# Kernel optimization log

Measured on AMD Instinct MI355X. Metric: run time of the kernel, lower is better.

The kernel has to match this reference:

```python
import jax, jax.numpy as jnp
import numpy as np

B, S, H, D = 8, 1024, 1024, 64

def setup_inputs() -> dict:
    key = jax.random.key(0)
    ks = jax.random.split(key, 8)
    return {
        "query": jax.random.normal(ks[0], (B, S, H), jnp.float32),
        "key": jax.random.normal(ks[1], (B, S, H), jnp.float32),
        "value": jax.random.normal(ks[2], (B, S, H), jnp.float32),
        "Wq": jax.random.normal(ks[3], (H, D), jnp.float32) * 0.02,
        "bq": jnp.zeros((D,), jnp.float32),
        "Wk": jax.random.normal(ks[4], (H, D), jnp.float32) * 0.02,
        "bk": jnp.zeros((D,), jnp.float32),
        "Wv": jax.random.normal(ks[5], (H, D), jnp.float32) * 0.02,
        "bv": jnp.zeros((D,), jnp.float32),
        "k_bias_matrix": jax.random.normal(ks[6], (S, S, D), jnp.float32) * 0.02,
        "v_bias_matrix": jax.random.normal(ks[7], (S, S, D), jnp.float32) * 0.02,
        "mask": jnp.ones((B, S), jnp.int32),
    }

def reference(query, key, value, Wq, bq, Wk, bk, Wv, bv, k_bias_matrix, v_bias_matrix, mask):
    # Linear projections: [B,S,H] -> [B,S,D]
    q = query @ Wq + bq
    k = key @ Wk + bk
    v = value @ Wv + bv
    # Standard content score + Shaw relative-position key bias score
    attn_1 = jnp.einsum('bqd,bkd->bqk', q, k)
    attn_2 = jnp.einsum('bqd,qkd->bqk', q, k_bias_matrix)
    scores = (attn_1 + attn_2) / jnp.sqrt(jnp.float32(D))
    scores = jnp.where(mask[:, None, :] == 0, jnp.float32(-1e9), scores)
    w = jax.nn.softmax(scores, axis=-1)  # [B,S,S]
    values_1 = jnp.einsum('bqk,bkd->bqd', w, v)
    values_2 = jnp.einsum('bqk,qkd->bqd', w, v_bias_matrix)
    return values_1 + values_2
```

## Files before the change

### kernel.cpp

```cpp
#include <hip/hip_runtime.h>
#include <hip/hip_bf16.h>
#include <cstdint>
#include <cstddef>

#define NB 8
#define NS 1024
#define NH 1024
#define ND 64

typedef __attribute__((ext_vector_type(8))) short bf8_t;
typedef __attribute__((ext_vector_type(4))) float f32x4;
typedef __attribute__((ext_vector_type(4))) short short4v;

__device__ __forceinline__ short f2bfs(float x) {
    union { __hip_bfloat16 h; short s; } u;
    u.h = __float2bfloat16(x);
    return u.s;
}
__device__ __forceinline__ float bf2f(unsigned short h) {
    return __uint_as_float(((unsigned int)h) << 16);
}
__device__ __forceinline__ bf8_t pack_bf8(float4 a, float4 b) {
    bf8_t r;
    r[0] = f2bfs(a.x); r[1] = f2bfs(a.y); r[2] = f2bfs(a.z); r[3] = f2bfs(a.w);
    r[4] = f2bfs(b.x); r[5] = f2bfs(b.y); r[6] = f2bfs(b.z); r[7] = f2bfs(b.w);
    return r;
}

#define QP_OFF  0
#define KP_OFF  524288
#define VPT_OFF 1048576
#define S1_OFF  1572864
#define WT_OFF  9961472

__global__ __launch_bounds__(256, 8) void wcvt_kernel(
    const float* __restrict__ Wq, const float* __restrict__ Wk,
    const float* __restrict__ Wv, short* __restrict__ wt)
{
    const int p = blockIdx.y;
    const int n = blockIdx.x;
    const float* W = (p == 0) ? Wq : (p == 1) ? Wk : Wv;
    const int k0 = threadIdx.x * 4;
    short4v pk;
    #pragma unroll
    for (int i = 0; i < 4; ++i) pk[i] = f2bfs(W[(size_t)(k0 + i) * ND + n]);
    *(short4v*)&wt[((size_t)p * 64 + n) * 1024 + k0] = pk;
}

__global__ __launch_bounds__(256, 3) void proj_kernel(
    const float* __restrict__ qin, const float* __restrict__ kin, const float* __restrict__ vin,
    const short* __restrict__ wt,
    const float* __restrict__ bq, const float* __restrict__ bk, const float* __restrict__ bv,
    short* __restrict__ ws_s)
{
    __shared__ float red[2][16][68];

    const int p = blockIdx.y;
    const float* A    = (p == 0) ? qin : (p == 1) ? kin : vin;
    const float* bias = (p == 0) ? bq  : (p == 1) ? bk  : bv;

    const int t = threadIdx.x;
    const int wv = t >> 6, l = t & 63, lr = l & 15, lg = l >> 4;
    const int rt = wv >> 1, kh = wv & 1;
    const int rw = blockIdx.x * 32 + rt * 16;

    const short* wtp = wt + ((size_t)p * 64) * 1024 + kh * 512;
    const float* ab  = A + (size_t)(rw + lr) * NH + kh * 512;

    f32x4 acc[4];
    #pragma unroll
    for (int n = 0; n < 4; ++n) acc[n] = (f32x4){0.f, 0.f, 0.f, 0.f};

    #pragma unroll 2
    for (int ch = 0; ch < 4; ++ch) {
        #pragma unroll
        for (int s = 0; s < 4; ++s) {
            const int off = ch * 128 + s * 32 + lg * 8;
            bf8_t af = pack_bf8(*(const float4*)&ab[off], *(const float4*)&ab[off + 4]);
            #pragma unroll
            for (int n = 0; n < 4; ++n) {
                bf8_t bf = *(const bf8_t*)&wtp[(size_t)(n * 16 + lr) * 1024 + off];
                acc[n] = __builtin_amdgcn_mfma_f32_16x16x32_bf16(af, bf, acc[n], 0, 0, 0);
            }
        }
    }

    if (kh) {
        #pragma unroll
        for (int n = 0; n < 4; ++n)
            #pragma unroll
            for (int r = 0; r < 4; ++r)
                red[rt][lg * 4 + r][n * 16 + lr] = acc[n][r];
    }
    __syncthreads();
    if (!kh) {
        if (p < 2) {
            short* dst = ws_s + ((p == 0) ? QP_OFF : KP_OFF);
            const float sc = (p == 0) ? 0.125f : 1.0f;
            #pragma unroll
            for (int n = 0; n < 4; ++n) {
                const float bs = bias[n * 16 + lr];
                #pragma unroll
                for (int r = 0; r < 4; ++r) {
                    float v = acc[n][r] + red[rt][lg * 4 + r][n * 16 + lr] + bs;
                    dst[(size_t)(rw + lg * 4 + r) * ND + n * 16 + lr] = f2bfs(v * sc);
                }
            }
        } else {
            short* vpT = ws_s + VPT_OFF;
            const int b = rw >> 10;
            const int sbase = (rw & 1023) + lg * 4;
            #pragma unroll
            for (int n = 0; n < 4; ++n) {
                const float bs = bias[n * 16 + lr];
                short4v pk;
                #pragma unroll
                for (int r = 0; r < 4; ++r)
                    pk[r] = f2bfs(acc[n][r] + red[rt][lg * 4 + r][n * 16 + lr] + bs);
                *(short4v*)&vpT[((size_t)b * 64 + n * 16 + lr) * NS + sbase] = pk;
            }
        }
    }
}

__global__ __launch_bounds__(256, 4) void scores_c_kernel(
    const short* __restrict__ ws_s, short* __restrict__ s1)
{
    const short* qp = ws_s + QP_OFF;
    const short* kp = ws_s + KP_OFF;
    const int t = threadIdx.x;
    const int wv = t >> 6, l = t & 63, lr = l & 15, lg = l >> 4;
    const int q0 = blockIdx.y * 16;
    const int k0 = blockIdx.x * 64 + wv * 16;

    #pragma unroll
    for (int b = 0; b < 8; ++b) {
        const short* ap = &qp[((size_t)b * NS + q0 + lr) * ND + lg * 8];
        const short* bp = &kp[((size_t)b * NS + k0 + lr) * ND + lg * 8];
        bf8_t a0 = *(const bf8_t*)ap;
        bf8_t a1 = *(const bf8_t*)(ap + 32);
        bf8_t b0 = *(const bf8_t*)bp;
        bf8_t b1 = *(const bf8_t*)(bp + 32);
        f32x4 acc = {0.f, 0.f, 0.f, 0.f};
        acc = __builtin_amdgcn_mfma_f32_16x16x32_bf16(a0, b0, acc, 0, 0, 0);
        acc = __builtin_amdgcn_mfma_f32_16x16x32_bf16(a1, b1, acc, 0, 0, 0);
        #pragma unroll
        for (int r = 0; r < 4; ++r)
            s1[((size_t)b * NS + q0 + lg * 4 + r) * NS + k0 + lr] = f2bfs(acc[r]);
    }
}

__global__ __launch_bounds__(256, 4) void mega_kernel(
    const short* __restrict__ ws_s,
    short* __restrict__ s1,
    const float* __restrict__ kbias,
    const float* __restrict__ vbias,
    const int* __restrict__ mask,
    float* __restrict__ out)
{
    __shared__ __align__(16) short Sb[8][1032];
    __shared__ __align__(16) short WtT[8 * 16 * 64];

    const short* qp = ws_s + QP_OFF;
    const int q = blockIdx.x, t = threadIdx.x;
    const int wv = t >> 6, l = t & 63, lr = l & 15, lg = l >> 4;

    {
        const bf8_t aq0 = *(const bf8_t*)&qp[((size_t)(lr & 7) * NS + q) * ND + lg * 8];
        const bf8_t aq1 = *(const bf8_t*)&qp[((size_t)(lr & 7) * NS + q) * ND + 32 + lg * 8];
        const float* kbq = kbias + (size_t)q * NS * ND;

        #pragma unroll 4
        for (int it = 0; it < 16; ++it) {
            const int k0 = wv * 256 + it * 16;
            const float* kb = &kbq[(size_t)(k0 + lr) * ND + lg * 8];
            bf8_t b0 = pack_bf8(*(const float4*)kb, *(const float4*)(kb + 4));
            bf8_t b1 = pack_bf8(*(const float4*)(kb + 32), *(const float4*)(kb + 36));
            f32x4 acc = {0.f, 0.f, 0.f, 0.f};
            acc = __builtin_amdgcn_mfma_f32_16x16x32_bf16(aq0, b0, acc, 0, 0, 0);
            acc = __builtin_amdgcn_mfma_f32_16x16x32_bf16(aq1, b1, acc, 0, 0, 0);
            if (lg < 2) {
                #pragma unroll
                for (int r = 0; r < 4; ++r)
                    Sb[lg * 4 + r][k0 + lr] = f2bfs(acc[r]);
            }
        }
    }
    __syncthreads();

    {
        const int b = t >> 5, idx = t & 31;
        const int kk = idx * 32;
        short* r1 = s1 + ((size_t)b * NS + q) * NS + kk;
        const int* mb = mask + b * NS + kk;
        const float LOG2E = 1.4426950408889634f;

        float x[32];
        float m = -3.0e38f;
        #pragma unroll
        for (int c = 0; c < 4; ++c) {
            uint4 a4 = *(const uint4*)&r1[8 * c];
            uint4 b4 = *(const uint4*)&Sb[b][kk + 8 * c];
            int4 m0 = *(const int4*)&mb[8 * c];
            int4 m1 = *(const int4*)&mb[8 * c + 4];
            const unsigned short* ap = (const unsigned short*)&a4;
            const unsigned short* bp = (const unsigned short*)&b4;
            const int* mp = (const int*)&m0;
            const int* mq = (const int*)&m1;
            #pragma unroll
            for (int j = 0; j < 8; ++j) {
                float v = bf2f(ap[j]) + bf2f(bp[j]);
                const int mvv = (j < 4) ? mp[j] : mq[j - 4];
                v = (mvv == 0) ? -1e9f : v;
                x[8 * c + j] = v;
                m = fmaxf(m, v);
            }
        }
        #pragma unroll
        for (int off = 1; off < 32; off <<= 1) m = fmaxf(m, __shfl_xor(m, off, 32));

        float lsum = 0.f;
        #pragma unroll
        for (int j = 0; j < 32; ++j) { x[j] = exp2f((x[j] - m) * LOG2E); lsum += x[j]; }
        #pragma unroll
        for (int off = 1; off < 32; off <<= 1) lsum += __shfl_xor(lsum, off, 32);
        const float il = 1.0f / fmaxf(lsum, 1e-30f);

        unsigned short wv16[32];
        #pragma unroll
        for (int j = 0; j < 32; ++j) wv16[j] = (unsigned short)f2bfs(x[j] * il);

        #pragma unroll
        for (int c = 0; c < 4; ++c)
            *(uint4*)&r1[8 * c] = *(const uint4*)&wv16[8 * c];

        const int K = idx >> 1;
        #pragma unroll
        for (int G = 0; G < 4; ++G) {
            const int g = (idx & 1) * 4 + G;
            *(uint4*)&WtT[((size_t)b * 16 + K) * 64 + ((g ^ (K & 7)) << 3)] =
                *(const uint4*)&wv16[G * 8];
        }
    }
    __syncthreads();

    float* otile = (float*)&Sb[0][0];
    {
        const int kq = l >> 4, dq = l & 15;
        const int K4 = wv * 4 + kq;
        const int swz = K4 & 7;
        const int kbase = wv * 256 + kq * 64;
        const float* vbq = vbias + (size_t)q * NS * ND;

        float4 av[8];
        #pragma unroll
        for (int b = 0; b < 8; ++b) av[b] = make_float4(0.f, 0.f, 0.f, 0.f);

        for (int g = 0; g < 8; ++g) {
            uint4 wreg[8];
            #pragma unroll
            for (int b = 0; b < 8; ++b)
                wreg[b] = *(const uint4*)&WtT[((size_t)b * 16 + K4) * 64 + ((g ^ swz) << 3)];
            #pragma unroll
            for (int j = 0; j < 8; ++j) {
                const int k = kbase + g * 8 + j;
                const float4 vb = *(const float4*)&vbq[(size_t)k * ND + 4 * dq];
                #pragma unroll
                for (int b = 0; b < 8; ++b) {
                    const unsigned int word = ((const unsigned int*)&wreg[b])[j >> 1];
                    const float wgt = (j & 1) ? __uint_as_float(word & 0xffff0000u)
                                              : __uint_as_float(word << 16);
                    av[b].x += wgt * vb.x; av[b].y += wgt * vb.y;
                    av[b].z += wgt * vb.z; av[b].w += wgt * vb.w;
                }
            }
        }
        #pragma unroll
        for (int b = 0; b < 8; ++b) {
            #pragma unroll
            for (int off = 16; off <= 32; off <<= 1) {
                av[b].x += __shfl_xor(av[b].x, off, 64);
                av[b].y += __shfl_xor(av[b].y, off, 64);
                av[b].z += __shfl_xor(av[b].z, off, 64);
                av[b].w += __shfl_xor(av[b].w, off, 64);
            }
        }
        if (l < 16) {
            #pragma unroll
            for (int b = 0; b < 8; ++b)
                *(float4*)&otile[((size_t)wv * 8 + b) * 64 + 4 * l] = av[b];
        }
    }
    __syncthreads();

    if (t < 128) {
        const int b = t >> 4, dd = (t & 15) * 4;
        float4 s = make_float4(0.f, 0.f, 0.f, 0.f);
        #pragma unroll
        for (int w4 = 0; w4 < 4; ++w4) {
            float4 r = *(const float4*)&otile[((size_t)w4 * 8 + b) * 64 + dd];
            s.x += r.x; s.y += r.y; s.z += r.z; s.w += r.w;
        }
        *(float4*)&out[((size_t)b * NS + q) * ND + dd] = s;
    }
}

__global__ __launch_bounds__(256, 4) void v1_kernel(
    const short* __restrict__ ws_s, const short* __restrict__ w,
    float* __restrict__ out)
{
    const short* vpT = ws_s + VPT_OFF;
    const int t = threadIdx.x, wv = t >> 6, l = t & 63, lr = l & 15, lg = l >> 4;
    const int b = blockIdx.y;
    const int q0 = blockIdx.x * 8;

    f32x4 acc[4];
    #pragma unroll
    for (int j = 0; j < 4; ++j) acc[j] = (f32x4){0.f, 0.f, 0.f, 0.f};

    const short* arow = &w[((size_t)b * NS + q0 + (lr & 7)) * NS + lg * 8];
    const short* brow = &vpT[((size_t)b * ND + wv * 16 + lr) * NS + lg * 8];
    #pragma unroll 8
    for (int ch = 0; ch < 32; ++ch) {
        bf8_t a  = *(const bf8_t*)(arow + ch * 32);
        bf8_t bb = *(const bf8_t*)(brow + ch * 32);
        acc[ch & 3] = __builtin_amdgcn_mfma_f32_16x16x32_bf16(a, bb, acc[ch & 3], 0, 0, 0);
    }
    f32x4 s;
    #pragma unroll
    for (int r = 0; r < 4; ++r) s[r] = acc[0][r] + acc[1][r] + acc[2][r] + acc[3][r];

    if (lg < 2) {
        #pragma unroll
        for (int r = 0; r < 4; ++r) {
            float* op = &out[((size_t)b * NS + q0 + lg * 4 + r) * ND + wv * 16 + lr];
            *op = *op + s[r];
        }
    }
}

extern "C" void kernel_launch(void* const* d_in, const int* in_sizes, int n_in,
                              void* d_out, int out_size, void* d_ws, size_t ws_size,
                              hipStream_t stream) {
    (void)in_sizes; (void)n_in; (void)out_size; (void)ws_size;
    const float* query = (const float*)d_in[0];
    const float* key   = (const float*)d_in[1];
    const float* value = (const float*)d_in[2];
    const float* Wq    = (const float*)d_in[3];
    const float* bq    = (const float*)d_in[4];
    const float* Wk    = (const float*)d_in[5];
    const float* bk    = (const float*)d_in[6];
    const float* Wv    = (const float*)d_in[7];
    const float* bv    = (const float*)d_in[8];
    const float* kbias = (const float*)d_in[9];
    const float* vbias = (const float*)d_in[10];
    const int*   mask  = (const int*)d_in[11];
    short* ws_s = (short*)d_ws;
    short* s1 = ws_s + S1_OFF;
    short* wt = ws_s + WT_OFF;
    float* outp = (float*)d_out;

    wcvt_kernel<<<dim3(64, 3), 256, 0, stream>>>(Wq, Wk, Wv, wt);
    proj_kernel<<<dim3(256, 3), 256, 0, stream>>>(query, key, value, wt, bq, bk, bv, ws_s);
    scores_c_kernel<<<dim3(16, 64), 256, 0, stream>>>(ws_s, s1);
    mega_kernel<<<1024, 256, 0, stream>>>(ws_s, s1, kbias, vbias, mask, outp);
    v1_kernel<<<dim3(128, 8), 256, 0, stream>>>(ws_s, s1, outp);
}
```

Baseline: 211.4 us.

## Store softmax weights row-major in LDS and use full MFMA rows in v1

The mega kernel now writes the normalized bf16 weights to a plain per-batch row-major LDS array instead of a swizzled transposed layout. The v_bias accumulation loop is restructured to read 4 weights per batch and 4 v_bias rows per step, with each quarter-wave handling interleaved k groups. This changes the global access pattern on v_bias and the LDS read pattern, which may introduce bank conflicts. Separately, v1_kernel now processes 16 query rows per block, using all 16 MFMA rows instead of duplicating 8, which halves the grid and lowers the launch-bounds occupancy hint.

After: 195.2 us. 1.08x faster.

```diff
diff --git a/kernel.cpp b/kernel.cpp
--- a/kernel.cpp
+++ b/kernel.cpp
@@ -159,7 +159,7 @@
     float* __restrict__ out)
 {
     __shared__ __align__(16) short Sb[8][1032];
-    __shared__ __align__(16) short WtT[8 * 16 * 64];
+    __shared__ __align__(16) short Wt[8][1024];
 
     const short* qp = ws_s + QP_OFF;
     const int q = blockIdx.x, t = threadIdx.x;
@@ -231,15 +231,9 @@
         for (int j = 0; j < 32; ++j) wv16[j] = (unsigned short)f2bfs(x[j] * il);
 
         #pragma unroll
-        for (int c = 0; c < 4; ++c)
-            *(uint4*)&r1[8 * c] = *(const uint4*)&wv16[8 * c];
-
-        const int K = idx >> 1;
-        #pragma unroll
-        for (int G = 0; G < 4; ++G) {
-            const int g = (idx & 1) * 4 + G;
-            *(uint4*)&WtT[((size_t)b * 16 + K) * 64 + ((g ^ (K & 7)) << 3)] =
-                *(const uint4*)&wv16[G * 8];
+        for (int c = 0; c < 4; ++c) {
+            *(uint4*)&r1[8 * c]         = *(const uint4*)&wv16[8 * c];
+            *(uint4*)&Wt[b][kk + 8 * c] = *(const uint4*)&wv16[8 * c];
         }
     }
     __syncthreads();
@@ -247,31 +241,29 @@
     float* otile = (float*)&Sb[0][0];
     {
         const int kq = l >> 4, dq = l & 15;
-        const int K4 = wv * 4 + kq;
-        const int swz = K4 & 7;
-        const int kbase = wv * 256 + kq * 64;
+        const int kw = wv * 256;
         const float* vbq = vbias + (size_t)q * NS * ND;
 
         float4 av[8];
         #pragma unroll
         for (int b = 0; b < 8; ++b) av[b] = make_float4(0.f, 0.f, 0.f, 0.f);
 
-        for (int g = 0; g < 8; ++g) {
-            uint4 wreg[8];
-            #pragma unroll
-            for (int b = 0; b < 8; ++b)
-                wreg[b] = *(const uint4*)&WtT[((size_t)b * 16 + K4) * 64 + ((g ^ swz) << 3)];
-            #pragma unroll
-            for (int j = 0; j < 8; ++j) {
-                const int k = kbase + g * 8 + j;
-                const float4 vb = *(const float4*)&vbq[(size_t)k * ND + 4 * dq];
+        for (int i = 0; i < 16; ++i) {
+            const int kb = kw + i * 16 + kq * 4;
+            short4v w4[8];
+            #pragma unroll
+            for (int b = 0; b < 8; ++b) w4[b] = *(const short4v*)&Wt[b][kb];
+            float4 vb[4];
+            #pragma unroll
+            for (int j = 0; j < 4; ++j)
+                vb[j] = *(const float4*)&vbq[(size_t)(kb + j) * ND + 4 * dq];
+            #pragma unroll
+            for (int j = 0; j < 4; ++j) {
                 #pragma unroll
                 for (int b = 0; b < 8; ++b) {
-                    const unsigned int word = ((const unsigned int*)&wreg[b])[j >> 1];
-                    const float wgt = (j & 1) ? __uint_as_float(word & 0xffff0000u)
-                                              : __uint_as_float(word << 16);
-                    av[b].x += wgt * vb.x; av[b].y += wgt * vb.y;
-                    av[b].z += wgt * vb.z; av[b].w += wgt * vb.w;
+                    const float wgt = bf2f((unsigned short)w4[b][j]);
+                    av[b].x += wgt * vb[j].x; av[b].y += wgt * vb[j].y;
+                    av[b].z += wgt * vb[j].z; av[b].w += wgt * vb[j].w;
                 }
             }
         }
@@ -305,20 +297,20 @@
     }
 }
 
-__global__ __launch_bounds__(256, 4) void v1_kernel(
+__global__ __launch_bounds__(256, 2) void v1_kernel(
     const short* __restrict__ ws_s, const short* __restrict__ w,
     float* __restrict__ out)
 {
     const short* vpT = ws_s + VPT_OFF;
     const int t = threadIdx.x, wv = t >> 6, l = t & 63, lr = l & 15, lg = l >> 4;
     const int b = blockIdx.y;
-    const int q0 = blockIdx.x * 8;
+    const int q0 = blockIdx.x * 16;
 
     f32x4 acc[4];
     #pragma unroll
     for (int j = 0; j < 4; ++j) acc[j] = (f32x4){0.f, 0.f, 0.f, 0.f};
 
-    const short* arow = &w[((size_t)b * NS + q0 + (lr & 7)) * NS + lg * 8];
+    const short* arow = &w[((size_t)b * NS + q0 + lr) * NS + lg * 8];
     const short* brow = &vpT[((size_t)b * ND + wv * 16 + lr) * NS + lg * 8];
     #pragma unroll 8
     for (int ch = 0; ch < 32; ++ch) {
@@ -330,12 +322,10 @@
     #pragma unroll
     for (int r = 0; r < 4; ++r) s[r] = acc[0][r] + acc[1][r] + acc[2][r] + acc[3][r];
 
-    if (lg < 2) {
-        #pragma unroll
-        for (int r = 0; r < 4; ++r) {
-            float* op = &out[((size_t)b * NS + q0 + lg * 4 + r) * ND + wv * 16 + lr];
-            *op = *op + s[r];
-        }
+    #pragma unroll
+    for (int r = 0; r < 4; ++r) {
+        float* op = &out[((size_t)b * NS + q0 + lg * 4 + r) * ND + wv * 16 + lr];
+        *op = *op + s[r];
     }
 }
 
@@ -364,5 +354,5 @@
     proj_kernel<<<dim3(256, 3), 256, 0, stream>>>(query, key, value, wt, bq, bk, bv, ws_s);
     scores_c_kernel<<<dim3(16, 64), 256, 0, stream>>>(ws_s, s1);
     mega_kernel<<<1024, 256, 0, stream>>>(ws_s, s1, kbias, vbias, mask, outp);
-    v1_kernel<<<dim3(128, 8), 256, 0, stream>>>(ws_s, s1, outp);
-}
+    v1_kernel<<<dim3(64, 8), 256, 0, stream>>>(ws_s, s1, outp);
+}
```
